# Performance work log

Hardware: AMD Instinct MI355X
Metric: run time of the kernel (lower is better)

The kernel has to match this reference:

```python
import jax, jax.numpy as jnp
import numpy as np

B, S, D = 4, 2048, 768

def setup_inputs() -> dict:
    key = jax.random.key(0)
    ks = jax.random.split(key, 7)
    scale = 1.0 / np.sqrt(D)
    x = jax.random.normal(ks[0], (B, S, D), dtype=jnp.float32)
    Wq = jax.random.uniform(ks[1], (D, D), jnp.float32, -scale, scale)
    bq = jax.random.uniform(ks[2], (D,), jnp.float32, -scale, scale)
    Wk = jax.random.uniform(ks[3], (D, D), jnp.float32, -scale, scale)
    bk = jax.random.uniform(ks[4], (D,), jnp.float32, -scale, scale)
    Wv = jax.random.uniform(ks[5], (D, D), jnp.float32, -scale, scale)
    bv = jax.random.uniform(ks[6], (D,), jnp.float32, -scale, scale)
    return {"x": x, "Wq": Wq, "bq": bq, "Wk": Wk, "bk": bk, "Wv": Wv, "bv": bv}

def reference(x, Wq, bq, Wk, bk, Wv, bv):
    d = x.shape[-1]
    q = jnp.einsum('bsd,de->bse', x, Wq) + bq
    k = jnp.einsum('bsd,de->bse', x, Wk) + bk
    v = jnp.einsum('bsd,de->bse', x, Wv) + bv
    scores = jnp.einsum('bqd,bkd->bqk', q, k) / jnp.sqrt(jnp.asarray(d, x.dtype))
    attn = jax.nn.softmax(scores, axis=-1)  # [B,S,S]
    return jnp.einsum('bqk,bkd->bqd', attn, v)
```

## Files before the change

kernel.cpp:

```cpp
#include <hip/hip_runtime.h>
#include <hip/hip_bf16.h>


typedef __attribute__((ext_vector_type(8))) short short8;
typedef __attribute__((ext_vector_type(4))) short short4v;
typedef __attribute__((ext_vector_type(4))) float float4v;

static constexpr int B_ = 4, S_ = 2048, D_ = 768;
static constexpr int MS = B_ * S_;

__device__ inline short f2bf(float f) {
  __hip_bfloat16 h = __float2bfloat16(f);
  union { __hip_bfloat16 h; short s; } u; u.h = h; return u.s;
}
__device__ inline float bf2f(short s) {
  union { unsigned int u; float f; } c;
  c.u = ((unsigned int)(unsigned short)s) << 16; return c.f;
}

typedef const __attribute__((address_space(1))) unsigned int g_u32;
typedef __attribute__((address_space(3))) unsigned int l_u32;

__device__ __forceinline__ void glds16(const short* g, short* l) {
  __builtin_amdgcn_global_load_lds((g_u32*)g, (l_u32*)l, 16, 0, 0);
}

__global__ __launch_bounds__(256)
void cast_f32_bf16(const float* __restrict__ x, short* __restrict__ y, int n) {
  int i = (blockIdx.x * 256 + threadIdx.x) * 4;
  if (i + 3 < n) {
    float4v v = *(const float4v*)(x + i);
    short4v o;
    o.x = f2bf(v.x); o.y = f2bf(v.y); o.z = f2bf(v.z); o.w = f2bf(v.w);
    *(short4v*)(y + i) = o;
  }
}

__global__ void transpose_cast_w(const float* __restrict__ W0, const float* __restrict__ W1,
                                 const float* __restrict__ W2,
                                 short* __restrict__ T0, short* __restrict__ T1,
                                 short* __restrict__ T2) {
  const float* W = blockIdx.z == 0 ? W0 : (blockIdx.z == 1 ? W1 : W2);
  short* T = blockIdx.z == 0 ? T0 : (blockIdx.z == 1 ? T1 : T2);
  __shared__ float tile[32][33];
  int bx = blockIdx.x * 32, by = blockIdx.y * 32;
  int tx = threadIdx.x, ty = threadIdx.y;
  for (int r = ty; r < 32; r += 8)
    tile[r][tx] = W[(by + r) * D_ + bx + tx];
  __syncthreads();
  for (int r = ty; r < 32; r += 8)
    T[(bx + r) * D_ + by + tx] = f2bf(tile[tx][r]);
}

template<int EPI, int TM, int TN>
__global__ __launch_bounds__(256)
void gemm_bt(const short* __restrict__ A, const short* __restrict__ Bt,
             void* __restrict__ C0v, short* __restrict__ C1, short* __restrict__ C2,
             const float* __restrict__ bias0, const float* __restrict__ bias1,
             const float* __restrict__ bias2,
             int K, int lda, int ldb, int ldc,
             long sA, long sB, long sC, float scale) {
  constexpr int BMv = TM * 32, BNv = TN * 32;
  const int b = blockIdx.z;
  A += (long)b * sA;
  Bt += (long)b * sB;
  float* Cf = (float*)C0v + (long)b * sC;
  short* Cs = (short*)C0v + (long)b * sC;

  __shared__ short As[BMv * 64];
  __shared__ short Bs[BNv * 64];

  const int t = threadIdx.x;
  const int wave = t >> 6, lane = t & 63;
  const int lane16 = lane & 15, q = lane >> 4;
  const int m0 = blockIdx.y * BMv, n0 = blockIdx.x * BNv;
  const int wm = (wave >> 1) * (TM * 16), wn = (wave & 1) * (TN * 16);
  const int rsub = lane >> 3;
  const int g = (lane & 7) ^ rsub;

  auto stage = [&](int kk) {
#pragma unroll
    for (int i = wave; i < BMv / 8; i += 4)
      glds16(A + (long)(m0 + i * 8 + rsub) * lda + kk + g * 8, &As[i * 512]);
#pragma unroll
    for (int i = wave; i < BNv / 8; i += 4)
      glds16(Bt + (long)(n0 + i * 8 + rsub) * ldb + kk + g * 8, &Bs[i * 512]);
  };

  stage(0);

  float4v acc[TM][TN];
#pragma unroll
  for (int i = 0; i < TM; i++)
#pragma unroll
    for (int j = 0; j < TN; j++) acc[i][j] = {0.f, 0.f, 0.f, 0.f};

  float4v acc_rs[TM];
#pragma unroll
  for (int i = 0; i < TM; i++) acc_rs[i] = {0.f, 0.f, 0.f, 0.f};
  short8 ones;
#pragma unroll
  for (int e = 0; e < 8; e++) ones[e] = (short)0x3F80;

  for (int k0 = 0; k0 < K; k0 += 64) {
    __syncthreads();

    short8 af[2][TM], bfr[2][TN];
#pragma unroll
    for (int s = 0; s < 2; s++) {
#pragma unroll
      for (int i = 0; i < TM; i++) {
        int R = wm + i * 16 + lane16;
        af[s][i] = *(const short8*)&As[R * 64 + (((s * 4 + q) ^ (R & 7)) * 8)];
      }
#pragma unroll
      for (int j = 0; j < TN; j++) {
        int R = wn + j * 16 + lane16;
        bfr[s][j] = *(const short8*)&Bs[R * 64 + (((s * 4 + q) ^ (R & 7)) * 8)];
      }
    }
    __syncthreads();

    if (k0 + 64 < K) stage(k0 + 64);

#pragma unroll
    for (int s = 0; s < 2; s++) {
#pragma unroll
      for (int i = 0; i < TM; i++) {
#pragma unroll
        for (int j = 0; j < TN; j++)
          acc[i][j] = __builtin_amdgcn_mfma_f32_16x16x32_bf16(af[s][i], bfr[s][j], acc[i][j], 0, 0, 0);
        if (EPI == 3)
          acc_rs[i] = __builtin_amdgcn_mfma_f32_16x16x32_bf16(af[s][i], ones, acc_rs[i], 0, 0, 0);
      }
    }
  }

#pragma unroll
  for (int i = 0; i < TM; i++) {
    int mrow = m0 + wm + i * 16 + q * 4;
    if (EPI == 0) {
#pragma unroll
      for (int j = 0; j < TN; j++) {
        int ncol = n0 + wn + j * 16 + lane16;
        if (ncol < 1536) {
          short* dst = ncol < 768 ? Cs : C1;
          const float* bs = ncol < 768 ? bias0 : bias1;
          int c = ncol < 768 ? ncol : ncol - 768;
#pragma unroll
          for (int rr = 0; rr < 4; rr++)
            dst[(long)(mrow + rr) * 768 + c] = f2bf(acc[i][j][rr] + bs[c]);
        } else {
          int e = ncol - 1536;
          float bv = bias2[e];
          short4v o;
#pragma unroll
          for (int rr = 0; rr < 4; rr++) o[rr] = f2bf(acc[i][j][rr] + bv);
          *(short4v*)&C2[(long)e * MS + mrow] = o;
        }
      }
    } else if (EPI == 2) {
#pragma unroll
      for (int j = 0; j < TN; j++) {
        int ncol = n0 + wn + j * 16 + lane16;
#pragma unroll
        for (int rr = 0; rr < 4; rr++)
          Cs[(long)(mrow + rr) * ldc + ncol] = f2bf(__expf(acc[i][j][rr] * scale));
      }
    } else {
#pragma unroll
      for (int rr = 0; rr < 4; rr++) {
        float inv = 1.0f / acc_rs[i][rr];
#pragma unroll
        for (int j = 0; j < TN; j++) {
          int ncol = n0 + wn + j * 16 + lane16;
          Cf[(long)(mrow + rr) * ldc + ncol] = acc[i][j][rr] * inv;
        }
      }
    }
  }
}

extern "C" void kernel_launch(void* const* d_in, const int* in_sizes, int n_in,
                              void* d_out, int out_size, void* d_ws, size_t ws_size,
                              hipStream_t stream) {
  const float* x  = (const float*)d_in[0];
  const float* Wq = (const float*)d_in[1];
  const float* bq = (const float*)d_in[2];
  const float* Wk = (const float*)d_in[3];
  const float* bk = (const float*)d_in[4];
  const float* Wv = (const float*)d_in[5];
  const float* bv = (const float*)d_in[6];
  float* out = (float*)d_out;

  short* Xb  = (short*)d_ws;
  short* WqT = Xb + (long)MS * D_;
  short* WkT = WqT + (long)D_ * D_;
  short* WvT = WkT + (long)D_ * D_;
  short* Qb  = WvT + (long)D_ * D_;
  short* Kb  = Qb + (long)MS * D_;
  short* Vt  = Kb + (long)MS * D_;
  short* Es  = Vt + (long)MS * D_;

  cast_f32_bf16<<<(MS * D_) / 1024, 256, 0, stream>>>(x, Xb, MS * D_);
  transpose_cast_w<<<dim3(24, 24, 3), dim3(32, 8), 0, stream>>>(Wq, Wk, Wv, WqT, WkT, WvT);

  gemm_bt<0, 4, 4><<<dim3(2304 / 128, MS / 128, 1), 256, 0, stream>>>(
      Xb, WqT, Qb, Kb, Vt, bq, bk, bv,
      D_, D_, D_, D_, 0, 0, 0, 1.0f);
  gemm_bt<2, 4, 4><<<dim3(S_ / 128, S_ / 128, B_), 256, 0, stream>>>(
      Qb, Kb, Es, nullptr, nullptr, nullptr, nullptr, nullptr,
      D_, D_, D_, S_,
      (long)S_ * D_, (long)S_ * D_, (long)S_ * S_, 1.0f / sqrtf((float)D_));
  gemm_bt<3, 4, 4><<<dim3(D_ / 128, S_ / 128, B_), 256, 0, stream>>>(
      Es, Vt, out, nullptr, nullptr, nullptr, nullptr, nullptr,
      S_, S_, MS, D_,
      (long)S_ * S_, (long)S_, (long)S_ * D_, 1.0f);
}
```

Before: 201.9 us.

## Load GEMM fragments directly from global memory instead of LDS staging

Removes the LDS tile staging (global_load_lds plus swizzled shared reads and two barriers per k-step) and has each lane load its MFMA A/B fragments straight from global memory with 16-byte loads. This removes the barrier synchronisation and the LDS traffic. In exchange, the A and B tiles are no longer shared between waves through LDS, so each is fetched from global memory once per wave that uses it. The fetches are also strided row reads that depend on cache hits, and there is no prefetch overlap across k-steps.

New measurement: 418.4 us. +107.2%, slower.

```diff
diff --git a/kernel.cpp b/kernel.cpp
--- a/kernel.cpp
+++ b/kernel.cpp
@@ -16,13 +16,6 @@
 __device__ inline float bf2f(short s) {
   union { unsigned int u; float f; } c;
   c.u = ((unsigned int)(unsigned short)s) << 16; return c.f;
-}
-
-typedef const __attribute__((address_space(1))) unsigned int g_u32;
-typedef __attribute__((address_space(3))) unsigned int l_u32;
-
-__device__ __forceinline__ void glds16(const short* g, short* l) {
-  __builtin_amdgcn_global_load_lds((g_u32*)g, (l_u32*)l, 16, 0, 0);
 }
 
 __global__ __launch_bounds__(256)
@@ -60,34 +53,26 @@
              const float* __restrict__ bias2,
              int K, int lda, int ldb, int ldc,
              long sA, long sB, long sC, float scale) {
-  constexpr int BMv = TM * 32, BNv = TN * 32;
   const int b = blockIdx.z;
   A += (long)b * sA;
   Bt += (long)b * sB;
   float* Cf = (float*)C0v + (long)b * sC;
   short* Cs = (short*)C0v + (long)b * sC;
 
-  __shared__ short As[BMv * 64];
-  __shared__ short Bs[BNv * 64];
-
   const int t = threadIdx.x;
   const int wave = t >> 6, lane = t & 63;
   const int lane16 = lane & 15, q = lane >> 4;
-  const int m0 = blockIdx.y * BMv, n0 = blockIdx.x * BNv;
+  const int m0 = blockIdx.y * (TM * 32), n0 = blockIdx.x * (TN * 32);
   const int wm = (wave >> 1) * (TM * 16), wn = (wave & 1) * (TN * 16);
-  const int rsub = lane >> 3;
-  const int g = (lane & 7) ^ rsub;
 
-  auto stage = [&](int kk) {
+  const short* Ar[TM];
+  const short* Br[TN];
 #pragma unroll
-    for (int i = wave; i < BMv / 8; i += 4)
-      glds16(A + (long)(m0 + i * 8 + rsub) * lda + kk + g * 8, &As[i * 512]);
+  for (int i = 0; i < TM; i++)
+    Ar[i] = A + (long)(m0 + wm + i * 16 + lane16) * lda + q * 8;
 #pragma unroll
-    for (int i = wave; i < BNv / 8; i += 4)
-      glds16(Bt + (long)(n0 + i * 8 + rsub) * ldb + kk + g * 8, &Bs[i * 512]);
-  };
-
-  stage(0);
+  for (int j = 0; j < TN; j++)
+    Br[j] = Bt + (long)(n0 + wn + j * 16 + lane16) * ldb + q * 8;
 
   float4v acc[TM][TN];
 #pragma unroll
@@ -103,36 +88,31 @@
   for (int e = 0; e < 8; e++) ones[e] = (short)0x3F80;
 
   for (int k0 = 0; k0 < K; k0 += 64) {
-    __syncthreads();
-
-    short8 af[2][TM], bfr[2][TN];
+    short8 af0[TM], bf0[TN], af1[TM], bf1[TN];
 #pragma unroll
-    for (int s = 0; s < 2; s++) {
+    for (int i = 0; i < TM; i++) af0[i] = *(const short8*)(Ar[i] + k0);
 #pragma unroll
-      for (int i = 0; i < TM; i++) {
-        int R = wm + i * 16 + lane16;
-        af[s][i] = *(const short8*)&As[R * 64 + (((s * 4 + q) ^ (R & 7)) * 8)];
-      }
+    for (int j = 0; j < TN; j++) bf0[j] = *(const short8*)(Br[j] + k0);
 #pragma unroll
-      for (int j = 0; j < TN; j++) {
-        int R = wn + j * 16 + lane16;
-        bfr[s][j] = *(const short8*)&Bs[R * 64 + (((s * 4 + q) ^ (R & 7)) * 8)];
-      }
-    }
-    __syncthreads();
-
-    if (k0 + 64 < K) stage(k0 + 64);
+    for (int i = 0; i < TM; i++) af1[i] = *(const short8*)(Ar[i] + k0 + 32);
+#pragma unroll
+    for (int j = 0; j < TN; j++) bf1[j] = *(const short8*)(Br[j] + k0 + 32);
 
 #pragma unroll
-    for (int s = 0; s < 2; s++) {
+    for (int i = 0; i < TM; i++) {
 #pragma unroll
-      for (int i = 0; i < TM; i++) {
+      for (int j = 0; j < TN; j++)
+        acc[i][j] = __builtin_amdgcn_mfma_f32_16x16x32_bf16(af0[i], bf0[j], acc[i][j], 0, 0, 0);
+      if (EPI == 3)
+        acc_rs[i] = __builtin_amdgcn_mfma_f32_16x16x32_bf16(af0[i], ones, acc_rs[i], 0, 0, 0);
+    }
 #pragma unroll
-        for (int j = 0; j < TN; j++)
-          acc[i][j] = __builtin_amdgcn_mfma_f32_16x16x32_bf16(af[s][i], bfr[s][j], acc[i][j], 0, 0, 0);
-        if (EPI == 3)
-          acc_rs[i] = __builtin_amdgcn_mfma_f32_16x16x32_bf16(af[s][i], ones, acc_rs[i], 0, 0, 0);
-      }
+    for (int i = 0; i < TM; i++) {
+#pragma unroll
+      for (int j = 0; j < TN; j++)
+        acc[i][j] = __builtin_amdgcn_mfma_f32_16x16x32_bf16(af1[i], bf1[j], acc[i][j], 0, 0, 0);
+      if (EPI == 3)
+        acc_rs[i] = __builtin_amdgcn_mfma_f32_16x16x32_bf16(af1[i], ones, acc_rs[i], 0, 0, 0);
     }
   }
 
```
